# Performance work log

Hardware: AMD Instinct MI355X
Metric: run time of the kernel (lower is better)

## Reference

```python
import jax, jax.numpy as jnp
import numpy as np

B, N, E, DIN = 2048, 38, 4, 9
H0, H1, L0 = 256, 256, 512
EPS = 1e-5
_mask_np = np.ones((N, DIN), np.float32)
_mask_np[np.arange(0, N, 2), :] = 0.0
MASK = jnp.asarray(_mask_np)  # (N, DIN); masked rows zeroed


def _bn_relu(h, g, b):
    # h: (B, N, 1, D); BatchNorm2d(N) normalizes over (batch, H=1, W=D) per node channel
    mu = jnp.mean(h, axis=(0, 2, 3), keepdims=True)
    var = jnp.var(h, axis=(0, 2, 3), keepdims=True)  # biased var, as torch BN
    h = (h - mu) * jax.lax.rsqrt(var + EPS) * g[None, :, None, None] + b[None, :, None, None]
    return jax.nn.relu(h)


def _gconv(adj, nodes, Ws, bs, We, be):
    # adj: (B, E, N, N); nodes: (B, N, 1, Din)
    out = Ws.shape[0]
    hs = nodes @ Ws.T + bs  # self term: (B, N, 1, out)
    m = (nodes @ We.T + be).reshape(nodes.shape[0], N, out, E)
    hr = jnp.einsum('bemn,bnce->bmc', adj, m)  # relational aggregation
    return hs + hr[:, :, None, :]


def _forward(adj, x, cWs0, cbs0, cWe0, cbe0, cg0, cb0, cWs1, cbs1, cWe1, cbe1, cg1, cb1, lW0, lb0, lg0, lbb0, fW, fb):
    masked_x = MASK * x
    h = masked_x[:, :, None, :]
    h = _bn_relu(_gconv(adj, h, cWs0, cbs0, cWe0, cbe0), cg0, cb0)
    h = _bn_relu(_gconv(adj, h, cWs1, cbs1, cWe1, cbe1), cg1, cb1)
    h = _bn_relu(h @ lW0.T + lb0, lg0, lbb0)
    h = (h @ fW.T + fb)[:, :, 0, :]  # (B, N, 2*DIN)
    s_logits, t = h[..., :DIN], h[..., DIN:]
    s = jax.nn.sigmoid(s_logits)
    out = masked_x + (1.0 - MASK) * (x + t) * s
    logdet = jnp.sum(jax.nn.log_sigmoid(s_logits).reshape(x.shape[0], -1), axis=1)
    return out, logdet


def setup_inputs() -> dict:
    key = jax.random.key(0)
    ks = jax.random.split(key, 8)
    rn = lambda k, shape: jax.random.normal(ks[k], shape, jnp.float32) * 0.1
    return {
        'adj': jax.random.uniform(ks[0], (B, E, N, N), jnp.float32),
        'x': jax.random.normal(ks[1], (B, N, DIN), jnp.float32),
        'cWs0': rn(2, (H0, DIN)), 'cbs0': jnp.zeros((H0,), jnp.float32),
        'cWe0': rn(3, (H0 * E, DIN)), 'cbe0': jnp.zeros((H0 * E,), jnp.float32),
        'cg0': jnp.ones((N,), jnp.float32), 'cb0': jnp.zeros((N,), jnp.float32),
        'cWs1': rn(4, (H1, H0)), 'cbs1': jnp.zeros((H1,), jnp.float32),
        'cWe1': rn(5, (H1 * E, H0)), 'cbe1': jnp.zeros((H1 * E,), jnp.float32),
        'cg1': jnp.ones((N,), jnp.float32), 'cb1': jnp.zeros((N,), jnp.float32),
        'lW0': rn(6, (L0, H1)), 'lb0': jnp.zeros((L0,), jnp.float32),
        'lg0': jnp.ones((N,), jnp.float32), 'lbb0': jnp.zeros((N,), jnp.float32),
        'fW': rn(7, (2 * DIN, L0)), 'fb': jnp.zeros((2 * DIN,), jnp.float32),
    }


def reference(adj, x, cWs0, cbs0, cWe0, cbe0, cg0, cb0, cWs1, cbs1, cWe1, cbe1, cg1, cb1, lW0, lb0, lg0, lbb0, fW, fb):
    return _forward(adj, x, cWs0, cbs0, cWe0, cbe0, cg0, cb0, cWs1, cbs1, cWe1, cbe1, cg1, cb1, lW0, lb0, lg0, lbb0, fW, fb)
```

## Files before the change

### kernel.cpp

```cpp
#include <hip/hip_runtime.h>
#include <hip/hip_bf16.h>
#include <math.h>

#define B_   2048
#define N_   38
#define E_   4
#define DIN_ 9
#define H0_  256
#define H1_  256
#define L0_  512
#define M_   (B_ * N_)

typedef short bf16x8 __attribute__((ext_vector_type(8)));
typedef float f32x4 __attribute__((ext_vector_type(4)));

struct __align__(8) bf4 { __hip_bfloat16 x, y, z, w; };

__device__ __forceinline__ float b2f(unsigned short u) {
  return __uint_as_float((unsigned)u << 16);
}
__device__ __forceinline__ unsigned short f2b(float f) {
  __hip_bfloat16 h = __float2bfloat16(f);
  return *(unsigned short*)&h;
}
__device__ __forceinline__ float4 ld4v(const __hip_bfloat16* p) {
  bf4 v = *(const bf4*)p;
  return make_float4(__bfloat162float(v.x), __bfloat162float(v.y),
                     __bfloat162float(v.z), __bfloat162float(v.w));
}
__device__ __forceinline__ void st4v(__hip_bfloat16* p, float4 v) {
  bf4 o;
  o.x = __float2bfloat16(v.x); o.y = __float2bfloat16(v.y);
  o.z = __float2bfloat16(v.z); o.w = __float2bfloat16(v.w);
  *(bf4*)p = o;
}

static __device__ __forceinline__ float selc(const float4 v, int j) {
  return (j == 0) ? v.x : ((j == 1) ? v.y : ((j == 2) ? v.z : v.w));
}

__device__ __forceinline__ void fma_tile12(const float* __restrict__ zr, float4 w,
                                           float (&acc)[4][12]) {
#pragma unroll
  for (int l4 = 0; l4 < 3; ++l4) {
    float4 zv = *(const float4*)&zr[l4 * 4];
#pragma unroll
    for (int j = 0; j < 4; ++j) {
      float wj = selc(w, j);
      acc[j][l4 * 4 + 0] = fmaf(zv.x, wj, acc[j][l4 * 4 + 0]);
      acc[j][l4 * 4 + 1] = fmaf(zv.y, wj, acc[j][l4 * 4 + 1]);
      acc[j][l4 * 4 + 2] = fmaf(zv.z, wj, acc[j][l4 * 4 + 2]);
      acc[j][l4 * 4 + 3] = fmaf(zv.w, wj, acc[j][l4 * 4 + 3]);
    }
  }
}

__global__ void k_zero(float* __restrict__ p) { p[threadIdx.x] = 0.f; }

__global__ void k_build_w0(const float* __restrict__ Ws, const float* __restrict__ We,
                           float* __restrict__ WT) {
  int i = blockIdx.x * 256 + threadIdx.x;
  if (i >= 45 * 256) return;
  int r = i / 256, c = i % 256;
  float v;
  if (r < 9) v = Ws[c * 9 + r];
  else { int rr = r - 9; int e = rr / 9, f = rr % 9; v = We[(c * 4 + e) * 9 + f]; }
  WT[i] = v;
}

__global__ void k_build_wbig(const float* __restrict__ Ws, const float* __restrict__ We,
                             unsigned short* __restrict__ WT) {
  int i = blockIdx.x * 256 + threadIdx.x;
  if (i >= 1280 * 256) return;
  int j = i / 256, f = i % 256;
  float v;
  if (j < 256) v = Ws[j * 256 + f];
  else { int jj = j - 256; int e = jj >> 8, c = jj & 255; v = We[(c * 4 + e) * 256 + f]; }
  WT[i] = f2b(v);
}

__global__ void k_build_wl(const float* __restrict__ W, unsigned short* __restrict__ WT) {
  int i = blockIdx.x * 256 + threadIdx.x;
  if (i >= 512 * 256) return;
  WT[i] = f2b(W[i]);
}

__global__ void k_build_wf(const float* __restrict__ W, unsigned short* __restrict__ WT) {
  int i = blockIdx.x * 256 + threadIdx.x;
  if (i >= 32 * 512) return;
  int r = i / 512, k = i % 512;
  WT[i] = f2b(r < 18 ? W[r * 512 + k] : 0.f);
}

__global__ __launch_bounds__(256) void k_gconv0(
    const float* __restrict__ adj, const float* __restrict__ x,
    const float* __restrict__ WT, const float* __restrict__ bs,
    const float* __restrict__ be, __hip_bfloat16* __restrict__ g) {
  __shared__ __align__(16) float adjF[E_ * N_ * N_];
  __shared__ __align__(16) float xc[45 * 48];
  __shared__ __align__(16) float arow[E_ * 48];
  const int b = blockIdx.x, tid = threadIdx.x;
  const size_t abase = (size_t)b * (E_ * N_ * N_);
  for (int i = tid; i < E_ * N_ * N_; i += 256) adjF[i] = adj[abase + i];
  for (int i = tid; i < N_ * DIN_; i += 256) {
    int n = i / DIN_;
    float v = x[(size_t)b * (N_ * DIN_) + i];
    xc[(i % DIN_) * 48 + n] = (n & 1) ? v : 0.f;
  }
  __syncthreads();
  for (int i = tid; i < E_ * N_; i += 256) {
    int e = i / N_, m = i % N_;
    const float* ar = &adjF[(e * N_ + m) * N_];
    float s = 0.f;
    for (int n = 0; n < N_; ++n) s += ar[n];
    arow[e * 48 + m] = s;
  }
  for (int i = tid; i < 36 * N_; i += 256) {
    int m = i % N_, ef = i / N_;
    int e = ef / 9, f = ef % 9;
    const float* ar = &adjF[(e * N_ + m) * N_];
    float s = 0.f;
    for (int n = 0; n < N_; ++n) s += ar[n] * xc[f * 48 + n];
    xc[(9 + ef) * 48 + m] = s;
  }
  __syncthreads();
  const int cg = tid & 63, mg = tid >> 6;
  const int c0 = cg * 4, mb = mg * 12;
  float acc[4][12];
#pragma unroll
  for (int j = 0; j < 4; ++j) {
    float bsv = bs[c0 + j];
    float b0 = be[(c0 + j) * 4 + 0], b1 = be[(c0 + j) * 4 + 1];
    float b2 = be[(c0 + j) * 4 + 2], b3 = be[(c0 + j) * 4 + 3];
#pragma unroll
    for (int l = 0; l < 12; ++l) {
      int m = mb + l;
      acc[j][l] = bsv + arow[0 * 48 + m] * b0 + arow[1 * 48 + m] * b1 +
                  arow[2 * 48 + m] * b2 + arow[3 * 48 + m] * b3;
    }
  }
  for (int k = 0; k < 45; ++k) {
    float4 w = *(const float4*)&WT[k * 256 + c0];
    fma_tile12(&xc[k * 48 + mb], w, acc);
  }
#pragma unroll
  for (int l = 0; l < 12; ++l) {
    int m = mb + l;
    if (m < N_) {
      float4 o; o.x = acc[0][l]; o.y = acc[1][l]; o.z = acc[2][l]; o.w = acc[3][l];
      st4v(&g[((size_t)b * N_ + m) * H0_ + c0], o);
    }
  }
}

__global__ __launch_bounds__(256) void k_stats(const __hip_bfloat16* __restrict__ g, int C,
                                               float* __restrict__ st) {
  int n = blockIdx.x, s = blockIdx.y, tid = threadIdx.x;
  int C4 = C >> 2;
  float sum = 0.f, sq = 0.f;
  int per = 64 * C4;
  for (int j = tid; j < per; j += 256) {
    int bb = (s << 6) + j / C4, cc = j % C4;
    float4 v = ld4v(&g[((size_t)(bb * N_ + n) * C4 + cc) * 4]);
    sum += v.x + v.y + v.z + v.w;
    sq += v.x * v.x + v.y * v.y + v.z * v.z + v.w * v.w;
  }
  for (int off = 32; off; off >>= 1) {
    sum += __shfl_down(sum, off);
    sq += __shfl_down(sq, off);
  }
  __shared__ float rs[4], rq[4];
  int w = tid >> 6, l = tid & 63;
  if (!l) { rs[w] = sum; rq[w] = sq; }
  __syncthreads();
  if (!tid) {
    float S = 0.f, Q = 0.f;
    for (int i = 0; i < 4; ++i) { S += rs[i]; Q += rq[i]; }
    atomicAdd(&st[n * 2], S);
    atomicAdd(&st[n * 2 + 1], Q);
  }
}

__global__ __launch_bounds__(256) void k_prep2(
    unsigned short* __restrict__ g, const float* __restrict__ st,
    const float* __restrict__ gam, const float* __restrict__ bet) {
  size_t i = (size_t)blockIdx.x * 256 + threadIdx.x;
  int n = (int)((i >> 5) % N_);
  const float cnt = 2048.f * 256.f;
  float mu = st[n * 2] / cnt;
  float var = st[n * 2 + 1] / cnt - mu * mu;
  float a = rsqrtf(var + 1e-5f) * gam[n];
  float bb = bet[n] - mu * a;
  uint4 u = *((const uint4*)g + i);
  uint4 o;
  unsigned* up = (unsigned*)&u;
  unsigned* op = (unsigned*)&o;
#pragma unroll
  for (int j = 0; j < 4; ++j) {
    float lo = b2f((unsigned short)(up[j] & 0xffff));
    float hi = b2f((unsigned short)(up[j] >> 16));
    lo = fmaxf(fmaf(lo, a, bb), 0.f);
    hi = fmaxf(fmaf(hi, a, bb), 0.f);
    op[j] = (unsigned)f2b(lo) | ((unsigned)f2b(hi) << 16);
  }
  *((uint4*)g + i) = o;
}

template <bool BIAS>
__global__ __launch_bounds__(512) void k_gemm(
    const unsigned short* __restrict__ A0, const unsigned short* __restrict__ Bw,
    const float* __restrict__ bias, unsigned short* __restrict__ Cout,
    int Cstride) {
  __shared__ __align__(16) unsigned short lA[128 * 32];
  __shared__ __align__(16) unsigned short lB[256 * 32];
  __shared__ float lbias[256];
  const int t = threadIdx.x;
  const int tileM = blockIdx.x, n_base = blockIdx.y * 256;
  if (BIAS && t < 256) lbias[t] = bias[n_base + t];
  const int w = t >> 6, L = t & 63;
  const int wr = w >> 2, wc = w & 3;
  const int lrow = L & 15, quad = L >> 4;
  const int srow = t >> 2, sseg = (t & 3) * 8;
  f32x4 acc[4][4];
#pragma unroll
  for (int mt = 0; mt < 4; ++mt)
#pragma unroll
    for (int nt = 0; nt < 4; ++nt) acc[mt][nt] = (f32x4){0.f, 0.f, 0.f, 0.f};

  for (int ki = 0; ki < 8; ++ki) {
    {
      const unsigned short* gp = A0 + (size_t)(tileM * 128 + srow) * 256 + ki * 32 + sseg;
      __builtin_amdgcn_global_load_lds(
          (const __attribute__((address_space(1))) void*)gp,
          (__attribute__((address_space(3))) void*)(lA + w * 512), 16, 0, 0);
    }
#pragma unroll
    for (int r = 0; r < 2; ++r) {
      const unsigned short* gp = Bw + (size_t)(n_base + r * 128 + srow) * 256 + ki * 32 + sseg;
      __builtin_amdgcn_global_load_lds(
          (const __attribute__((address_space(1))) void*)gp,
          (__attribute__((address_space(3))) void*)(lB + r * 4096 + w * 512), 16, 0, 0);
    }
    __syncthreads();
    bf16x8 af[4], bfr[4];
#pragma unroll
    for (int mt = 0; mt < 4; ++mt)
      af[mt] = *(const bf16x8*)&lA[(wr * 64 + mt * 16 + lrow) * 32 + quad * 8];
#pragma unroll
    for (int nt = 0; nt < 4; ++nt)
      bfr[nt] = *(const bf16x8*)&lB[(wc * 64 + nt * 16 + lrow) * 32 + quad * 8];
#pragma unroll
    for (int mt = 0; mt < 4; ++mt)
#pragma unroll
      for (int nt = 0; nt < 4; ++nt)
        acc[mt][nt] = __builtin_amdgcn_mfma_f32_16x16x32_bf16(af[mt], bfr[nt], acc[mt][nt], 0, 0, 0);
    __syncthreads();
  }
#pragma unroll
  for (int mt = 0; mt < 4; ++mt) {
#pragma unroll
    for (int reg = 0; reg < 4; ++reg) {
      const size_t row = (size_t)tileM * 128 + wr * 64 + mt * 16 + quad * 4 + reg;
#pragma unroll
      for (int nt = 0; nt < 4; ++nt) {
        const int lcol = wc * 64 + nt * 16 + lrow;
        float v = acc[mt][nt][reg];
        if (BIAS) v += lbias[lcol];
        Cout[row * Cstride + n_base + lcol] = f2b(v);
      }
    }
  }
}

__global__ __launch_bounds__(256) void k_hr(
    const float* __restrict__ adj, const unsigned short* __restrict__ Y,
    const float* __restrict__ bs, const float* __restrict__ be,
    unsigned short* __restrict__ h2, int b_base) {
  __shared__ __align__(16) unsigned short adjE[4 * 48 * 64];
  __shared__ __align__(16) unsigned short Ybt[256 * 72];
  __shared__ float arowS[4 * 48];
  const int t = threadIdx.x;
  const int bl = blockIdx.x, b = b_base + bl;
  for (int i = t; i < 4 * 48 * 64 / 8; i += 256) ((uint4*)adjE)[i] = make_uint4(0, 0, 0, 0);
#pragma unroll
  for (int n = 38; n < 64; ++n) Ybt[t * 72 + n] = 0;
  __syncthreads();
  for (int i = t; i < 4 * 38 * 38; i += 256) {
    int e = i / 1444, r = i % 1444, m = r / 38, n = r % 38;
    adjE[(e * 48 + m) * 64 + n] = f2b(adj[(size_t)b * 5776 + i]);
  }
  __syncthreads();
  if (t < 152) {
    int e = t / 38, m = t % 38;
    float s = 0.f;
    for (int n = 0; n < 38; ++n) s += b2f(adjE[(e * 48 + m) * 64 + n]);
    arowS[e * 48 + m] = s;
  }
  const int w = t >> 6, L = t & 63;
  const int lrow = L & 15, quad = L >> 4;
  f32x4 acc[3][4];
#pragma unroll
  for (int mt = 0; mt < 3; ++mt)
#pragma unroll
    for (int nt = 0; nt < 4; ++nt) acc[mt][nt] = (f32x4){0.f, 0.f, 0.f, 0.f};
#pragma unroll 1
  for (int e = 0; e < 4; ++e) {
    __syncthreads();
    {
      const unsigned short* yp = Y + (size_t)bl * 38 * 1280 + 256 + e * 256 + t;
#pragma unroll
      for (int n = 0; n < 38; ++n) Ybt[t * 72 + n] = yp[(size_t)n * 1280];
    }
    __syncthreads();
#pragma unroll
    for (int kk = 0; kk < 2; ++kk) {
      bf16x8 bb[4];
#pragma unroll
      for (int nt = 0; nt < 4; ++nt)
        bb[nt] = *(const bf16x8*)&Ybt[(w * 64 + nt * 16 + lrow) * 72 + kk * 32 + quad * 8];
#pragma unroll
      for (int mt = 0; mt < 3; ++mt) {
        bf16x8 aa = *(const bf16x8*)&adjE[(e * 48 + mt * 16 + lrow) * 64 + kk * 32 + quad * 8];
#pragma unroll
        for (int nt = 0; nt < 4; ++nt)
          acc[mt][nt] = __builtin_amdgcn_mfma_f32_16x16x32_bf16(aa, bb[nt], acc[mt][nt], 0, 0, 0);
      }
    }
  }
#pragma unroll
  for (int mt = 0; mt < 3; ++mt) {
#pragma unroll
    for (int reg = 0; reg < 4; ++reg) {
      const int m = mt * 16 + quad * 4 + reg;
      if (m < N_) {
        float a0 = arowS[0 * 48 + m], a1 = arowS[1 * 48 + m];
        float a2 = arowS[2 * 48 + m], a3 = arowS[3 * 48 + m];
#pragma unroll
        for (int nt = 0; nt < 4; ++nt) {
          const int col = w * 64 + nt * 16 + lrow;
          float hs = b2f(Y[(size_t)(bl * 38 + m) * 1280 + col]);
          float4 bev = *(const float4*)&be[col * 4];
          float v = acc[mt][nt][reg] + hs + bs[col] +
                    a0 * bev.x + a1 * bev.y + a2 * bev.z + a3 * bev.w;
          h2[((size_t)b * N_ + m) * 256 + col] = f2b(v);
        }
      }
    }
  }
}

__global__ __launch_bounds__(256) void k_final(
    const unsigned short* __restrict__ g2, const float* __restrict__ x,
    const unsigned short* __restrict__ Wfb, const float* __restrict__ fb,
    const float* __restrict__ st, const float* __restrict__ gam,
    const float* __restrict__ bet, float* __restrict__ out) {
  __shared__ __align__(16) unsigned short hA[48 * 520];
  __shared__ float lgS[48 * 20];
  __shared__ float aS[N_], bS[N_], fbS[20], red[4];
  const int b = blockIdx.x, tid = threadIdx.x;
  if (tid < N_) {
    const float cnt = 2048.f * 512.f;
    float mu = st[tid * 2] / cnt;
    float var = st[tid * 2 + 1] / cnt - mu * mu;
    float a = rsqrtf(var + 1e-5f) * gam[tid];
    aS[tid] = a;
    bS[tid] = bet[tid] - mu * a;
  }
  if (tid >= 64 && tid < 82) fbS[tid - 64] = fb[tid - 64];
  __syncthreads();
  for (int i = tid; i < N_ * 64; i += 256) {
    int n = i >> 6, seg = (i & 63) * 8;
    uint4 u = *(const uint4*)&g2[((size_t)b * N_ + n) * 512 + seg];
    float a = aS[n], bb = bS[n];
    float v[8];
    v[0] = b2f((unsigned short)(u.x & 0xffff)); v[1] = b2f((unsigned short)(u.x >> 16));
    v[2] = b2f((unsigned short)(u.y & 0xffff)); v[3] = b2f((unsigned short)(u.y >> 16));
    v[4] = b2f((unsigned short)(u.z & 0xffff)); v[5] = b2f((unsigned short)(u.z >> 16));
    v[6] = b2f((unsigned short)(u.w & 0xffff)); v[7] = b2f((unsigned short)(u.w >> 16));
#pragma unroll
    for (int j = 0; j < 8; ++j) v[j] = fmaxf(fmaf(v[j], a, bb), 0.f);
    uint4 o;
    o.x = (unsigned)f2b(v[0]) | ((unsigned)f2b(v[1]) << 16);
    o.y = (unsigned)f2b(v[2]) | ((unsigned)f2b(v[3]) << 16);
    o.z = (unsigned)f2b(v[4]) | ((unsigned)f2b(v[5]) << 16);
    o.w = (unsigned)f2b(v[6]) | ((unsigned)f2b(v[7]) << 16);
    *(uint4*)&hA[n * 520 + seg] = o;
  }
  for (int i = tid; i < 10 * 64; i += 256) {
    int n = 38 + (i >> 6), seg = (i & 63) * 8;
    *(uint4*)&hA[n * 520 + seg] = make_uint4(0, 0, 0, 0);
  }
  __syncthreads();
  const int w = tid >> 6, L = tid & 63;
  const int lrow = L & 15, quad = L >> 4;
  if (w < 3) {
    f32x4 acc0 = (f32x4){0.f, 0.f, 0.f, 0.f}, acc1 = (f32x4){0.f, 0.f, 0.f, 0.f};
#pragma unroll
    for (int ki = 0; ki < 16; ++ki) {
      bf16x8 af = *(const bf16x8*)&hA[(w * 16 + lrow) * 520 + ki * 32 + quad * 8];
      bf16x8 b0 = *(const bf16x8*)&Wfb[(size_t)lrow * 512 + ki * 32 + quad * 8];
      bf16x8 b1 = *(const bf16x8*)&Wfb[(size_t)(16 + lrow) * 512 + ki * 32 + quad * 8];
      acc0 = __builtin_amdgcn_mfma_f32_16x16x32_bf16(af, b0, acc0, 0, 0, 0);
      acc1 = __builtin_amdgcn_mfma_f32_16x16x32_bf16(af, b1, acc1, 0, 0, 0);
    }
#pragma unroll
    for (int reg = 0; reg < 4; ++reg) {
      int m = w * 16 + quad * 4 + reg;
      if (m < N_) {
        lgS[m * 20 + lrow] = acc0[reg] + fbS[lrow];
        if (lrow < 2) lgS[m * 20 + 16 + lrow] = acc1[reg] + fbS[16 + lrow];
      }
    }
  }
  __syncthreads();
  float ls = 0.f;
  for (int ii = tid; ii < 342; ii += 256) {
    int mm = ii / 9, d = ii % 9;
    float sl = lgS[mm * 20 + d];
    float tv = lgS[mm * 20 + 9 + d];
    float xv = x[((size_t)b * N_ + mm) * 9 + d];
    float sg = 1.f / (1.f + expf(-sl));
    float o = (mm & 1) ? xv : (xv + tv) * sg;
    out[((size_t)b * N_ + mm) * 9 + d] = o;
    ls += (sl >= 0.f) ? -log1pf(expf(-sl)) : (sl - log1pf(expf(sl)));
  }
#pragma unroll
  for (int off = 32; off; off >>= 1) ls += __shfl_down(ls, off);
  if (L == 0) red[w] = ls;
  __syncthreads();
  if (tid == 0) out[(size_t)B_ * 342 + b] = red[0] + red[1] + red[2] + red[3];
}

extern "C" void kernel_launch(void* const* d_in, const int* in_sizes, int n_in,
                              void* d_out, int out_size, void* d_ws, size_t ws_size,
                              hipStream_t stream) {
  (void)in_sizes; (void)n_in; (void)out_size; (void)ws_size;
  const float* adj  = (const float*)d_in[0];
  const float* x    = (const float*)d_in[1];
  const float* cWs0 = (const float*)d_in[2];
  const float* cbs0 = (const float*)d_in[3];
  const float* cWe0 = (const float*)d_in[4];
  const float* cbe0 = (const float*)d_in[5];
  const float* cg0  = (const float*)d_in[6];
  const float* cb0  = (const float*)d_in[7];
  const float* cWs1 = (const float*)d_in[8];
  const float* cbs1 = (const float*)d_in[9];
  const float* cWe1 = (const float*)d_in[10];
  const float* cbe1 = (const float*)d_in[11];
  const float* cg1  = (const float*)d_in[12];
  const float* cb1  = (const float*)d_in[13];
  const float* lW0  = (const float*)d_in[14];
  const float* lb0  = (const float*)d_in[15];
  const float* lg0  = (const float*)d_in[16];
  const float* lbb0 = (const float*)d_in[17];
  const float* fW   = (const float*)d_in[18];
  const float* fb   = (const float*)d_in[19];
  float* out = (float*)d_out;

  char* p = (char*)d_ws;
  float* stats = (float*)p;                     p += 1024;
  float* wt0   = (float*)p;                     p += 45 * 256 * 4;
  unsigned short* Wfb  = (unsigned short*)p;    p += 32 * 512 * 2;
  unsigned short* Wbig = (unsigned short*)p;    p += 1280 * 256 * 2;
  unsigned short* Wl   = (unsigned short*)p;    p += 512 * 256 * 2;
  unsigned short* g0   = (unsigned short*)p;    p += (size_t)M_ * 256 * 2;
  unsigned short* h2   = (unsigned short*)p;    p += (size_t)M_ * 256 * 2;
  unsigned short* big  = (unsigned short*)p;
  unsigned short* Ybuf = big;
  unsigned short* g2   = big;

  k_zero<<<1, 256, 0, stream>>>(stats);
  k_build_w0<<<45, 256, 0, stream>>>(cWs0, cWe0, wt0);
  k_build_wbig<<<1280, 256, 0, stream>>>(cWs1, cWe1, Wbig);
  k_build_wl<<<512, 256, 0, stream>>>(lW0, Wl);
  k_build_wf<<<64, 256, 0, stream>>>(fW, Wfb);

  k_gconv0<<<2048, 256, 0, stream>>>(adj, x, wt0, cbs0, cbe0, (__hip_bfloat16*)g0);
  k_stats<<<dim3(38, 32), 256, 0, stream>>>((const __hip_bfloat16*)g0, 256, stats);
  k_prep2<<<M_ * 256 / 8 / 256, 256, 0, stream>>>(g0, stats, cg0, cb0);

  for (int hh = 0; hh < 2; ++hh) {
    k_gemm<false><<<dim3(304, 5), 512, 0, stream>>>(
        g0 + (size_t)hh * (M_ / 2) * 256, Wbig, (const float*)nullptr, Ybuf, 1280);
    k_hr<<<1024, 256, 0, stream>>>(adj, Ybuf, cbs1, cbe1, h2, hh * 1024);
  }
  k_stats<<<dim3(38, 32), 256, 0, stream>>>((const __hip_bfloat16*)h2, 256, stats + 76);
  k_prep2<<<M_ * 256 / 8 / 256, 256, 0, stream>>>(h2, stats + 76, cg1, cb1);

  k_gemm<true><<<dim3(608, 2), 512, 0, stream>>>(h2, Wl, lb0, g2, 512);
  k_stats<<<dim3(38, 32), 256, 0, stream>>>((const __hip_bfloat16*)g2, 512, stats + 152);

  k_final<<<2048, 256, 0, stream>>>(g2, x, Wfb, fb, stats + 152, lg0, lbb0, out);
}
```

Before: 516.8 us.

## Fuse BatchNorm statistics into producer epilogues and normalization into GEMM loads

Removes the standalone stats and normalize/ReLU passes. Each producing kernel (gconv0, hr, second GEMM) now accumulates per-node sum and sum-of-squares in shared memory and writes per-block partials. A small reduction kernel combines them deterministically, replacing global atomics and the zeroing kernel. The consuming GEMM applies the BN affine and ReLU while loading A through registers into LDS. This drops several full passes over the large activation buffers, but gives up the direct global-to-LDS load path and adds LDS atomics to the epilogues.

```diff
diff --git a/kernel.cpp b/kernel.cpp
--- a/kernel.cpp
+++ b/kernel.cpp
@@ -23,11 +23,6 @@
   __hip_bfloat16 h = __float2bfloat16(f);
   return *(unsigned short*)&h;
 }
-__device__ __forceinline__ float4 ld4v(const __hip_bfloat16* p) {
-  bf4 v = *(const bf4*)p;
-  return make_float4(__bfloat162float(v.x), __bfloat162float(v.y),
-                     __bfloat162float(v.z), __bfloat162float(v.w));
-}
 __device__ __forceinline__ void st4v(__hip_bfloat16* p, float4 v) {
   bf4 o;
   o.x = __float2bfloat16(v.x); o.y = __float2bfloat16(v.y);
@@ -54,8 +49,6 @@
     }
   }
 }
-
-__global__ void k_zero(float* __restrict__ p) { p[threadIdx.x] = 0.f; }
 
 __global__ void k_build_w0(const float* __restrict__ Ws, const float* __restrict__ We,
                            float* __restrict__ WT) {
@@ -92,14 +85,34 @@
   WT[i] = f2b(r < 18 ? W[r * 512 + k] : 0.f);
 }
 
+__global__ __launch_bounds__(256) void k_gred(const float* __restrict__ part, int nblk,
+                                              float* __restrict__ st) {
+  const int j = blockIdx.x, tid = threadIdx.x;
+  float s = 0.f;
+  for (int i = tid; i < nblk; i += 256) s += part[(size_t)i * 76 + j];
+#pragma unroll
+  for (int off = 32; off; off >>= 1) s += __shfl_down(s, off);
+  __shared__ float r[4];
+  if ((tid & 63) == 0) r[tid >> 6] = s;
+  __syncthreads();
+  if (tid == 0) {
+    float tot = r[0] + r[1] + r[2] + r[3];
+    if (j < 38) st[j * 2] = tot;
+    else st[(j - 38) * 2 + 1] = tot;
+  }
+}
+
 __global__ __launch_bounds__(256) void k_gconv0(
     const float* __restrict__ adj, const float* __restrict__ x,
     const float* __restrict__ WT, const float* __restrict__ bs,
-    const float* __restrict__ be, __hip_bfloat16* __restrict__ g) {
+    const float* __restrict__ be, __hip_bfloat16* __restrict__ g,
+    float* __restrict__ part) {
   __shared__ __align__(16) float adjF[E_ * N_ * N_];
   __shared__ __align__(16) float xc[45 * 48];
   __shared__ __align__(16) float arow[E_ * 48];
+  __shared__ float lsum[38], lsq[38];
   const int b = blockIdx.x, tid = threadIdx.x;
+  if (tid < 38) { lsum[tid] = 0.f; lsq[tid] = 0.f; }
   const size_t abase = (size_t)b * (E_ * N_ * N_);
   for (int i = tid; i < E_ * N_ * N_; i += 256) adjF[i] = adj[abase + i];
   for (int i = tid; i < N_ * DIN_; i += 256) {
@@ -149,90 +162,67 @@
     if (m < N_) {
       float4 o; o.x = acc[0][l]; o.y = acc[1][l]; o.z = acc[2][l]; o.w = acc[3][l];
       st4v(&g[((size_t)b * N_ + m) * H0_ + c0], o);
-    }
-  }
-}
-
-__global__ __launch_bounds__(256) void k_stats(const __hip_bfloat16* __restrict__ g, int C,
-                                               float* __restrict__ st) {
-  int n = blockIdx.x, s = blockIdx.y, tid = threadIdx.x;
-  int C4 = C >> 2;
-  float sum = 0.f, sq = 0.f;
-  int per = 64 * C4;
-  for (int j = tid; j < per; j += 256) {
-    int bb = (s << 6) + j / C4, cc = j % C4;
-    float4 v = ld4v(&g[((size_t)(bb * N_ + n) * C4 + cc) * 4]);
-    sum += v.x + v.y + v.z + v.w;
-    sq += v.x * v.x + v.y * v.y + v.z * v.z + v.w * v.w;
-  }
-  for (int off = 32; off; off >>= 1) {
-    sum += __shfl_down(sum, off);
-    sq += __shfl_down(sq, off);
-  }
-  __shared__ float rs[4], rq[4];
-  int w = tid >> 6, l = tid & 63;
-  if (!l) { rs[w] = sum; rq[w] = sq; }
-  __syncthreads();
-  if (!tid) {
-    float S = 0.f, Q = 0.f;
-    for (int i = 0; i < 4; ++i) { S += rs[i]; Q += rq[i]; }
-    atomicAdd(&st[n * 2], S);
-    atomicAdd(&st[n * 2 + 1], Q);
-  }
-}
-
-__global__ __launch_bounds__(256) void k_prep2(
-    unsigned short* __restrict__ g, const float* __restrict__ st,
-    const float* __restrict__ gam, const float* __restrict__ bet) {
-  size_t i = (size_t)blockIdx.x * 256 + threadIdx.x;
-  int n = (int)((i >> 5) % N_);
-  const float cnt = 2048.f * 256.f;
-  float mu = st[n * 2] / cnt;
-  float var = st[n * 2 + 1] / cnt - mu * mu;
-  float a = rsqrtf(var + 1e-5f) * gam[n];
-  float bb = bet[n] - mu * a;
-  uint4 u = *((const uint4*)g + i);
-  uint4 o;
-  unsigned* up = (unsigned*)&u;
-  unsigned* op = (unsigned*)&o;
-#pragma unroll
-  for (int j = 0; j < 4; ++j) {
-    float lo = b2f((unsigned short)(up[j] & 0xffff));
-    float hi = b2f((unsigned short)(up[j] >> 16));
-    lo = fmaxf(fmaf(lo, a, bb), 0.f);
-    hi = fmaxf(fmaf(hi, a, bb), 0.f);
-    op[j] = (unsigned)f2b(lo) | ((unsigned)f2b(hi) << 16);
-  }
-  *((uint4*)g + i) = o;
-}
-
-template <bool BIAS>
+      float s = o.x + o.y + o.z + o.w;
+      float q = o.x * o.x + o.y * o.y + o.z * o.z + o.w * o.w;
+      atomicAdd(&lsum[m], s);
+      atomicAdd(&lsq[m], q);
+    }
+  }
+  __syncthreads();
+  if (tid < 38) {
+    part[(size_t)b * 76 + tid] = lsum[tid];
+    part[(size_t)b * 76 + 38 + tid] = lsq[tid];
+  }
+}
+
+template <bool BIAS, bool STATS>
 __global__ __launch_bounds__(512) void k_gemm(
     const unsigned short* __restrict__ A0, const unsigned short* __restrict__ Bw,
-    const float* __restrict__ bias, unsigned short* __restrict__ Cout,
-    int Cstride) {
+    const float* __restrict__ bias, const float* __restrict__ stIn,
+    const float* __restrict__ gam, const float* __restrict__ bet, float cnt,
+    unsigned short* __restrict__ Cout, int Cstride, float* __restrict__ part) {
   __shared__ __align__(16) unsigned short lA[128 * 32];
   __shared__ __align__(16) unsigned short lB[256 * 32];
   __shared__ float lbias[256];
+  __shared__ float lsum[38], lsq[38];
   const int t = threadIdx.x;
   const int tileM = blockIdx.x, n_base = blockIdx.y * 256;
   if (BIAS && t < 256) lbias[t] = bias[n_base + t];
+  if (STATS && t < 38) { lsum[t] = 0.f; lsq[t] = 0.f; }
   const int w = t >> 6, L = t & 63;
   const int wr = w >> 2, wc = w & 3;
   const int lrow = L & 15, quad = L >> 4;
   const int srow = t >> 2, sseg = (t & 3) * 8;
+  const int nA = (tileM * 128 + srow) % 38;
+  float aC, bC;
+  {
+    float mu = stIn[nA * 2] / cnt;
+    float var = stIn[nA * 2 + 1] / cnt - mu * mu;
+    aC = rsqrtf(var + 1e-5f) * gam[nA];
+    bC = bet[nA] - mu * aC;
+  }
+  const unsigned short* aRow = A0 + (size_t)(tileM * 128 + srow) * 256 + sseg;
   f32x4 acc[4][4];
 #pragma unroll
   for (int mt = 0; mt < 4; ++mt)
 #pragma unroll
     for (int nt = 0; nt < 4; ++nt) acc[mt][nt] = (f32x4){0.f, 0.f, 0.f, 0.f};
 
+  uint4 u = *(const uint4*)aRow;
   for (int ki = 0; ki < 8; ++ki) {
+    uint4 un;
+    if (ki < 7) un = *(const uint4*)(aRow + (ki + 1) * 32);
     {
-      const unsigned short* gp = A0 + (size_t)(tileM * 128 + srow) * 256 + ki * 32 + sseg;
-      __builtin_amdgcn_global_load_lds(
-          (const __attribute__((address_space(1))) void*)gp,
-          (__attribute__((address_space(3))) void*)(lA + w * 512), 16, 0, 0);
+      uint4 o;
+      unsigned* up = (unsigned*)&u;
+      unsigned* op = (unsigned*)&o;
+#pragma unroll
+      for (int j = 0; j < 4; ++j) {
+        float lo = fmaxf(fmaf(b2f((unsigned short)(up[j] & 0xffff)), aC, bC), 0.f);
+        float hi = fmaxf(fmaf(b2f((unsigned short)(up[j] >> 16)), aC, bC), 0.f);
+        op[j] = (unsigned)f2b(lo) | ((unsigned)f2b(hi) << 16);
+      }
+      *(uint4*)&lA[srow * 32 + sseg] = o;
     }
 #pragma unroll
     for (int r = 0; r < 2; ++r) {
@@ -255,19 +245,36 @@
       for (int nt = 0; nt < 4; ++nt)
         acc[mt][nt] = __builtin_amdgcn_mfma_f32_16x16x32_bf16(af[mt], bfr[nt], acc[mt][nt], 0, 0, 0);
     __syncthreads();
+    u = un;
   }
 #pragma unroll
   for (int mt = 0; mt < 4; ++mt) {
 #pragma unroll
     for (int reg = 0; reg < 4; ++reg) {
       const size_t row = (size_t)tileM * 128 + wr * 64 + mt * 16 + quad * 4 + reg;
+      float sv = 0.f, qv = 0.f;
 #pragma unroll
       for (int nt = 0; nt < 4; ++nt) {
         const int lcol = wc * 64 + nt * 16 + lrow;
         float v = acc[mt][nt][reg];
         if (BIAS) v += lbias[lcol];
         Cout[row * Cstride + n_base + lcol] = f2b(v);
+        sv += v;
+        qv += v * v;
       }
+      if (STATS) {
+        int n = (int)(row % 38);
+        atomicAdd(&lsum[n], sv);
+        atomicAdd(&lsq[n], qv);
+      }
+    }
+  }
+  if (STATS) {
+    __syncthreads();
+    const int blk = blockIdx.y * gridDim.x + blockIdx.x;
+    if (t < 38) {
+      part[(size_t)blk * 76 + t] = lsum[t];
+      part[(size_t)blk * 76 + 38 + t] = lsq[t];
     }
   }
 }
@@ -275,12 +282,14 @@
 __global__ __launch_bounds__(256) void k_hr(
     const float* __restrict__ adj, const unsigned short* __restrict__ Y,
     const float* __restrict__ bs, const float* __restrict__ be,
-    unsigned short* __restrict__ h2, int b_base) {
+    unsigned short* __restrict__ h2, int b_base, float* __restrict__ part) {
   __shared__ __align__(16) unsigned short adjE[4 * 48 * 64];
   __shared__ __align__(16) unsigned short Ybt[256 * 72];
   __shared__ float arowS[4 * 48];
+  __shared__ float lsum[38], lsq[38];
   const int t = threadIdx.x;
   const int bl = blockIdx.x, b = b_base + bl;
+  if (t < 38) { lsum[t] = 0.f; lsq[t] = 0.f; }
   for (int i = t; i < 4 * 48 * 64 / 8; i += 256) ((uint4*)adjE)[i] = make_uint4(0, 0, 0, 0);
 #pragma unroll
   for (int n = 38; n < 64; ++n) Ybt[t * 72 + n] = 0;
@@ -335,6 +344,7 @@
       if (m < N_) {
         float a0 = arowS[0 * 48 + m], a1 = arowS[1 * 48 + m];
         float a2 = arowS[2 * 48 + m], a3 = arowS[3 * 48 + m];
+        float sv = 0.f, qv = 0.f;
 #pragma unroll
         for (int nt = 0; nt < 4; ++nt) {
           const int col = w * 64 + nt * 16 + lrow;
@@ -343,9 +353,18 @@
           float v = acc[mt][nt][reg] + hs + bs[col] +
                     a0 * bev.x + a1 * bev.y + a2 * bev.z + a3 * bev.w;
           h2[((size_t)b * N_ + m) * 256 + col] = f2b(v);
+          sv += v;
+          qv += v * v;
         }
+        atomicAdd(&lsum[m], sv);
+        atomicAdd(&lsq[m], qv);
       }
     }
+  }
+  __syncthreads();
+  if (t < 38) {
+    part[(size_t)b * 76 + t] = lsum[t];
+    part[(size_t)b * 76 + 38 + t] = lsq[t];
   }
 }
 
@@ -463,32 +482,38 @@
   unsigned short* Wfb  = (unsigned short*)p;    p += 32 * 512 * 2;
   unsigned short* Wbig = (unsigned short*)p;    p += 1280 * 256 * 2;
   unsigned short* Wl   = (unsigned short*)p;    p += 512 * 256 * 2;
+  float* part0 = (float*)p;                     p += 2048 * 76 * 4;
+  float* part1 = (float*)p;                     p += 2048 * 76 * 4;
+  float* part2 = (float*)p;                     p += 1216 * 76 * 4;
   unsigned short* g0   = (unsigned short*)p;    p += (size_t)M_ * 256 * 2;
   unsigned short* h2   = (unsigned short*)p;    p += (size_t)M_ * 256 * 2;
   unsigned short* big  = (unsigned short*)p;
   unsigned short* Ybuf = big;
   unsigned short* g2   = big;
 
-  k_zero<<<1, 256, 0, stream>>>(stats);
+  float* st0 = stats;
+  float* st1 = stats + 76;
+  float* st2 = stats + 152;
+
   k_build_w0<<<45, 256, 0, stream>>>(cWs0, cWe0, wt0);
   k_build_wbig<<<1280, 256, 0, stream>>>(cWs1, cWe1, Wbig);
   k_build_wl<<<512, 256, 0, stream>>>(lW0, Wl);
   k_build_wf<<<64, 256, 0, stream>>>(fW, Wfb);
 
-  k_gconv0<<<2048, 256, 0, stream>>>(adj, x, wt0, cbs0, cbe0, (__hip_bfloat16*)g0);
-  k_stats<<<dim3(38, 32), 256, 0, stream>>>((const __hip_bfloat16*)g0, 256, stats);
-  k_prep2<<<M_ * 256 / 8 / 256, 256, 0, stream>>>(g0, stats, cg0, cb0);
+  k_gconv0<<<2048, 256, 0, stream>>>(adj, x, wt0, cbs0, cbe0, (__hip_bfloat16*)g0, part0);
+  k_gred<<<76, 256, 0, stream>>>(part0, 2048, st0);
 
   for (int hh = 0; hh < 2; ++hh) {
-    k_gemm<false><<<dim3(304, 5), 512, 0, stream>>>(
-        g0 + (size_t)hh * (M_ / 2) * 256, Wbig, (const float*)nullptr, Ybuf, 1280);
-    k_hr<<<1024, 256, 0, stream>>>(adj, Ybuf, cbs1, cbe1, h2, hh * 1024);
-  }
-  k_stats<<<dim3(38, 32), 256, 0, stream>>>((const __hip_bfloat16*)h2, 256, stats + 76);
-  k_prep2<<<M_ * 256 / 8 / 256, 256, 0, stream>>>(h2, stats + 76, cg1, cb1);
-
-  k_gemm<true><<<dim3(608, 2), 512, 0, stream>>>(h2, Wl, lb0, g2, 512);
-  k_stats<<<dim3(38, 32), 256, 0, stream>>>((const __hip_bfloat16*)g2, 512, stats + 152);
-
-  k_final<<<2048, 256, 0, stream>>>(g2, x, Wfb, fb, stats + 152, lg0, lbb0, out);
-}
+    k_gemm<false, false><<<dim3(304, 5), 512, 0, stream>>>(
+        g0 + (size_t)hh * (M_ / 2) * 256, Wbig, (const float*)nullptr,
+        st0, cg0, cb0, 2048.f * 256.f, Ybuf, 1280, (float*)nullptr);
+    k_hr<<<1024, 256, 0, stream>>>(adj, Ybuf, cbs1, cbe1, h2, hh * 1024, part1);
+  }
+  k_gred<<<76, 256, 0, stream>>>(part1, 2048, st1);
+
+  k_gemm<true, true><<<dim3(608, 2), 512, 0, stream>>>(
+      h2, Wl, lb0, st1, cg1, cb1, 2048.f * 256.f, g2, 512, part2);
+  k_gred<<<76, 256, 0, stream>>>(part2, 1216, st2);
+
+  k_final<<<2048, 256, 0, stream>>>(g2, x, Wfb, fb, st2, lg0, lbb0, out);
+}
```

Result: slower. 651.9 us (+26.2%).
